# Optimization experiments

Measured on AMD Instinct MI355X. Metric: run time of the kernel, lower is better.

Reference implementation:

```python
import jax, jax.numpy as jnp
import numpy as np

N_TOKENS = 262144
D_IN = 128
D_OUT = 128
N_EXPERTS = 8


def setup_inputs() -> dict:
    key = jax.random.key(0)
    k1, k2, k3, k4 = jax.random.split(key, 4)
    x = jax.random.normal(k1, (N_TOKENS, D_IN), dtype=jnp.float32)
    split = jax.random.randint(k2, (N_TOKENS,), 0, N_EXPERTS, dtype=jnp.int64)
    # Per-expert Linear params (one "model" per unique split value).
    W = jax.random.normal(k3, (N_EXPERTS, D_IN, D_OUT), dtype=jnp.float32) / np.sqrt(D_IN)
    b = jax.random.normal(k4, (N_EXPERTS, D_OUT), dtype=jnp.float32)
    return {"x": x, "split": split, "W": W, "b": b}


def reference(x, split, W, b):
    # Original 'alone' path: gather rows per unique split value, apply
    # model[split_value], concat, then reorder via argsort of the gathered
    # indices. That composition is exactly a per-token expert apply:
    #   out[t] = x[t] @ W[split[t]] + b[split[t]]
    # Computed densely per expert (fixed shapes, jit-friendly), then select.
    y_all = jnp.einsum('nf,efg->eng', x, W) + b[:, None, :]  # [E, N, d_out]
    tok = jnp.arange(x.shape[0])
    return y_all[split, tok]  # [N, d_out]
```

## Files before the change

kernel.cpp:

```cpp
#include <hip/hip_runtime.h>


typedef __bf16 bf16x8 __attribute__((ext_vector_type(8)));
typedef unsigned short u16x8 __attribute__((ext_vector_type(8)));
typedef float f32x4 __attribute__((ext_vector_type(4)));

__device__ __forceinline__ unsigned short f2bf(float f) {
    unsigned u = __builtin_bit_cast(unsigned, f);
    u += 0x7FFFu + ((u >> 16) & 1u);
    return (unsigned short)(u >> 16);
}

__global__ void k_init(int* meta) {
    if (threadIdx.x < 16) meta[threadIdx.x] = 0;
}

__global__ void k_wt(const float* __restrict__ W, unsigned short* __restrict__ Wt) {
    __shared__ float T[16][132];
    int e = blockIdx.x >> 3;
    int g0 = (blockIdx.x & 7) << 4;
    const float* We = W + e * 128 * 128;
    #pragma unroll
    for (int i = 0; i < 2; ++i) {
        int idx = i * 256 + threadIdx.x;
        int f = idx >> 2, q = idx & 3;
        float4 v = *(const float4*)(We + f * 128 + g0 + q * 4);
        T[q * 4 + 0][f] = v.x; T[q * 4 + 1][f] = v.y;
        T[q * 4 + 2][f] = v.z; T[q * 4 + 3][f] = v.w;
    }
    __syncthreads();
    int g = threadIdx.x >> 4, fc = threadIdx.x & 15;
    u16x8 o;
    #pragma unroll
    for (int j = 0; j < 8; ++j) o[j] = f2bf(T[g][fc * 8 + j]);
    *(u16x8*)(Wt + ((e * 128 + g0 + g) * 128 + fc * 8)) = o;
}

__global__ void k_hist(const int* __restrict__ split, int* __restrict__ meta) {
    __shared__ int h[8];
    if (threadIdx.x < 8) h[threadIdx.x] = 0;
    __syncthreads();
    int t = blockIdx.x * 256 + threadIdx.x;
    atomicAdd(&h[split[t]], 1);
    __syncthreads();
    if (threadIdx.x < 8) atomicAdd(&meta[threadIdx.x], h[threadIdx.x]);
}

__global__ void k_scatter(const int* __restrict__ split, int* __restrict__ meta,
                          int* __restrict__ perm) {
    __shared__ int h[8], base[8];
    if (threadIdx.x < 8) h[threadIdx.x] = 0;
    __syncthreads();
    int t = blockIdx.x * 256 + threadIdx.x;
    int e = split[t];
    int r = atomicAdd(&h[e], 1);
    __syncthreads();
    if (threadIdx.x < 8)
        base[threadIdx.x] = atomicAdd(&meta[8 + threadIdx.x], h[threadIdx.x]);
    __syncthreads();
    int off = 0;
    #pragma unroll
    for (int ee = 0; ee < 8; ++ee) off += (ee < e) ? meta[ee] : 0;
    perm[off + base[e] + r] = t;
}

__global__ __launch_bounds__(512) void k_gemm(
    const float* __restrict__ x, const float* __restrict__ bias,
    const int* __restrict__ meta, const int* __restrict__ perm,
    const unsigned short* __restrict__ Wt, float* __restrict__ out) {

    int bid = blockIdx.x;
    int e = -1, tile = 0, cnt_e = 0, off_e = 0;
    int acc_t = 0, off = 0;
    #pragma unroll
    for (int ee = 0; ee < 8; ++ee) {
        int c = meta[ee];
        int t = (c + 255) >> 8;
        if (e < 0 && bid < acc_t + t) { e = ee; tile = bid - acc_t; cnt_e = c; off_e = off; }
        acc_t += t;
        off += c;
    }
    if (e < 0) return;

    __shared__ unsigned short Wl[16384];

    int tid = threadIdx.x;
    int lane = tid & 63;
    int w = tid >> 6;
    int l15 = lane & 15, lq = lane >> 4;

    const unsigned short* We = Wt + e * 16384;
    #pragma unroll
    for (int i = 0; i < 4; ++i) {
        int c = i * 512 + tid;
        int g = c >> 4, fc = c & 15;
        int slot = (g << 4) | (fc ^ (g & 7));
        *(u16x8*)(Wl + slot * 8) = *(const u16x8*)(We + c * 8);
    }

    bf16x8 afrag[2][4];
    #pragma unroll
    for (int i = 0; i < 2; ++i) {
        int p = tile * 256 + w * 32 + i * 16 + l15;
        int pp = p < cnt_e ? p : cnt_e - 1;
        int tok = perm[off_e + pp];
        const float* xr = x + (long)tok * 128 + lq * 8;
        #pragma unroll
        for (int kk = 0; kk < 4; ++kk) {
            float4 lo = *(const float4*)(xr + kk * 32);
            float4 hi = *(const float4*)(xr + kk * 32 + 4);
            u16x8 u;
            u[0] = f2bf(lo.x); u[1] = f2bf(lo.y); u[2] = f2bf(lo.z); u[3] = f2bf(lo.w);
            u[4] = f2bf(hi.x); u[5] = f2bf(hi.y); u[6] = f2bf(hi.z); u[7] = f2bf(hi.w);
            afrag[i][kk] = __builtin_bit_cast(bf16x8, u);
        }
    }

    __syncthreads();

    f32x4 acc[2][8];
    #pragma unroll
    for (int i = 0; i < 2; ++i)
        #pragma unroll
        for (int j = 0; j < 8; ++j) acc[i][j] = (f32x4){0.f, 0.f, 0.f, 0.f};

    #pragma unroll
    for (int kk = 0; kk < 4; ++kk) {
        #pragma unroll
        for (int j = 0; j < 8; ++j) {
            int g = j * 16 + l15;
            int fc = kk * 4 + lq;
            int slot = (g << 4) | (fc ^ (g & 7));
            bf16x8 b = *(const bf16x8*)(Wl + slot * 8);
            acc[0][j] = __builtin_amdgcn_mfma_f32_16x16x32_bf16(afrag[0][kk], b, acc[0][j], 0, 0, 0);
            acc[1][j] = __builtin_amdgcn_mfma_f32_16x16x32_bf16(afrag[1][kk], b, acc[1][j], 0, 0, 0);
        }
    }

    float bv[8];
    #pragma unroll
    for (int j = 0; j < 8; ++j) bv[j] = bias[e * 128 + j * 16 + l15];

    #pragma unroll
    for (int i = 0; i < 2; ++i) {
        #pragma unroll
        for (int r = 0; r < 4; ++r) {
            int p = tile * 256 + w * 32 + i * 16 + lq * 4 + r;
            if (p < cnt_e) {
                int tok = perm[off_e + p];
                float* o = out + (long)tok * 128 + l15;
                #pragma unroll
                for (int j = 0; j < 8; ++j) o[j * 16] = acc[i][j][r] + bv[j];
            }
        }
    }
}

extern "C" void kernel_launch(void* const* d_in, const int* in_sizes, int n_in,
                              void* d_out, int out_size, void* d_ws, size_t ws_size,
                              hipStream_t stream) {
    const float* x     = (const float*)d_in[0];
    const int*   split = (const int*)d_in[1];
    const float* W     = (const float*)d_in[2];
    const float* bias  = (const float*)d_in[3];
    float* out = (float*)d_out;

    int n = in_sizes[1];
    char* ws = (char*)d_ws;
    int* meta = (int*)ws;
    int* perm = (int*)(ws + 4096);
    unsigned short* Wt = (unsigned short*)(ws + 4096 + (size_t)n * 4);

    k_init<<<1, 64, 0, stream>>>(meta);
    k_wt<<<64, 256, 0, stream>>>(W, Wt);
    k_hist<<<n / 256, 256, 0, stream>>>(split, meta);
    k_scatter<<<n / 256, 256, 0, stream>>>(split, meta, perm);
    k_gemm<<<n / 256 + 8, 512, 0, stream>>>(x, bias, meta, perm, Wt, out);
}
```

Before: 96.12 us.

## Fuse histogram, scatter and GEMM into one per-tile kernel with local expert grouping

Replaces the global histogram/scatter/perm pipeline plus gathered GEMM with one kernel. Each block loads 256 contiguous tokens, groups them by expert in shared memory, and runs 16-row MFMA tiles per expert using weight fragments loaded from global memory. This removes three launches, the global atomics and the perm round-trip, and makes x reads coalesced. In exchange, each wave issues only one MFMA chain per 16-row tile, which raises per-tile overhead, and output writes become narrow scalar stores.

```diff
diff --git a/kernel.cpp b/kernel.cpp
--- a/kernel.cpp
+++ b/kernel.cpp
@@ -10,9 +10,8 @@
     u += 0x7FFFu + ((u >> 16) & 1u);
     return (unsigned short)(u >> 16);
 }
-
-__global__ void k_init(int* meta) {
-    if (threadIdx.x < 16) meta[threadIdx.x] = 0;
+__device__ __forceinline__ unsigned pack2(float a, float b) {
+    return (unsigned)f2bf(a) | ((unsigned)f2bf(b) << 16);
 }
 
 __global__ void k_wt(const float* __restrict__ W, unsigned short* __restrict__ Wt) {
@@ -36,121 +35,107 @@
     *(u16x8*)(Wt + ((e * 128 + g0 + g) * 128 + fc * 8)) = o;
 }
 
-__global__ void k_hist(const int* __restrict__ split, int* __restrict__ meta) {
-    __shared__ int h[8];
-    if (threadIdx.x < 8) h[threadIdx.x] = 0;
+#define NT 256
+
+__global__ __launch_bounds__(512) void k_fused(
+    const float* __restrict__ x, const int* __restrict__ split,
+    const float* __restrict__ bias, const unsigned short* __restrict__ Wt,
+    float* __restrict__ out) {
+
+    __shared__ unsigned short A[NT * 128];
+    __shared__ int hcnt[8], startE[8];
+    __shared__ int dest[NT], trow[NT];
+    __shared__ int exT[24], rbT[24], limT[24];
+    __shared__ int Tn;
+
+    const int tid = threadIdx.x;
+    const long t0 = (long)blockIdx.x * NT;
+
+    if (tid < 8) hcnt[tid] = 0;
     __syncthreads();
-    int t = blockIdx.x * 256 + threadIdx.x;
-    atomicAdd(&h[split[t]], 1);
+
+    float4 xv[16];
+    const float* xb = x + t0 * 128;
+    #pragma unroll
+    for (int rr = 0; rr < 16; ++rr)
+        xv[rr] = *(const float4*)(xb + (rr * 512 + tid) * 4);
+
+    int e = 0, rank = 0;
+    if (tid < NT) {
+        e = split[t0 + tid];
+        rank = atomicAdd(&hcnt[e], 1);
+    }
     __syncthreads();
-    if (threadIdx.x < 8) atomicAdd(&meta[threadIdx.x], h[threadIdx.x]);
-}
 
-__global__ void k_scatter(const int* __restrict__ split, int* __restrict__ meta,
-                          int* __restrict__ perm) {
-    __shared__ int h[8], base[8];
-    if (threadIdx.x < 8) h[threadIdx.x] = 0;
+    if (tid == 0) {
+        int acc = 0, T = 0;
+        for (int ee = 0; ee < 8; ++ee) {
+            int c = hcnt[ee];
+            startE[ee] = acc;
+            for (int k = 0; k < c; k += 16) {
+                exT[T] = ee; rbT[T] = acc + k;
+                limT[T] = (c - k < 16) ? (c - k) : 16; T++;
+            }
+            acc += c;
+        }
+        Tn = T;
+    }
     __syncthreads();
-    int t = blockIdx.x * 256 + threadIdx.x;
-    int e = split[t];
-    int r = atomicAdd(&h[e], 1);
+
+    if (tid < NT) {
+        int s = startE[e] + rank;
+        dest[tid] = s;
+        trow[s] = tid;
+    }
     __syncthreads();
-    if (threadIdx.x < 8)
-        base[threadIdx.x] = atomicAdd(&meta[8 + threadIdx.x], h[threadIdx.x]);
+
+    #pragma unroll
+    for (int rr = 0; rr < 16; ++rr) {
+        int c = rr * 512 + tid;
+        int row = c >> 5;
+        int s = dest[row];
+        int fc = (c & 31) >> 1;
+        int half = c & 1;
+        unsigned d0 = pack2(xv[rr].x, xv[rr].y);
+        unsigned d1 = pack2(xv[rr].z, xv[rr].w);
+        unsigned short* p = A + s * 128 + ((fc ^ (s & 7)) << 3) + half * 4;
+        *(uint2*)p = make_uint2(d0, d1);
+    }
     __syncthreads();
-    int off = 0;
-    #pragma unroll
-    for (int ee = 0; ee < 8; ++ee) off += (ee < e) ? meta[ee] : 0;
-    perm[off + base[e] + r] = t;
-}
 
-__global__ __launch_bounds__(512) void k_gemm(
-    const float* __restrict__ x, const float* __restrict__ bias,
-    const int* __restrict__ meta, const int* __restrict__ perm,
-    const unsigned short* __restrict__ Wt, float* __restrict__ out) {
+    const int lane = tid & 63, w = tid >> 6;
+    const int l15 = lane & 15, lq = lane >> 4;
+    const int T = Tn;
 
-    int bid = blockIdx.x;
-    int e = -1, tile = 0, cnt_e = 0, off_e = 0;
-    int acc_t = 0, off = 0;
-    #pragma unroll
-    for (int ee = 0; ee < 8; ++ee) {
-        int c = meta[ee];
-        int t = (c + 255) >> 8;
-        if (e < 0 && bid < acc_t + t) { e = ee; tile = bid - acc_t; cnt_e = c; off_e = off; }
-        acc_t += t;
-        off += c;
-    }
-    if (e < 0) return;
+    bf16x8 bfrag[4];
+    float bv = 0.f;
+    int preve = -1;
 
-    __shared__ unsigned short Wl[16384];
-
-    int tid = threadIdx.x;
-    int lane = tid & 63;
-    int w = tid >> 6;
-    int l15 = lane & 15, lq = lane >> 4;
-
-    const unsigned short* We = Wt + e * 16384;
-    #pragma unroll
-    for (int i = 0; i < 4; ++i) {
-        int c = i * 512 + tid;
-        int g = c >> 4, fc = c & 15;
-        int slot = (g << 4) | (fc ^ (g & 7));
-        *(u16x8*)(Wl + slot * 8) = *(const u16x8*)(We + c * 8);
-    }
-
-    bf16x8 afrag[2][4];
-    #pragma unroll
-    for (int i = 0; i < 2; ++i) {
-        int p = tile * 256 + w * 32 + i * 16 + l15;
-        int pp = p < cnt_e ? p : cnt_e - 1;
-        int tok = perm[off_e + pp];
-        const float* xr = x + (long)tok * 128 + lq * 8;
+    for (int tau = 0; tau < T; ++tau) {
+        int ee = exT[tau], rb = rbT[tau], lim = limT[tau];
+        if (ee != preve) {
+            preve = ee;
+            const unsigned short* Wb = Wt + ee * 16384 + (w * 16 + l15) * 128;
+            #pragma unroll
+            for (int kk = 0; kk < 4; ++kk)
+                bfrag[kk] = *(const bf16x8*)(Wb + (kk * 4 + lq) * 8);
+            bv = bias[ee * 128 + w * 16 + l15];
+        }
+        int srow = rb + l15;
+        srow = srow < NT - 1 ? srow : NT - 1;
+        f32x4 acc = {0.f, 0.f, 0.f, 0.f};
         #pragma unroll
         for (int kk = 0; kk < 4; ++kk) {
-            float4 lo = *(const float4*)(xr + kk * 32);
-            float4 hi = *(const float4*)(xr + kk * 32 + 4);
-            u16x8 u;
-            u[0] = f2bf(lo.x); u[1] = f2bf(lo.y); u[2] = f2bf(lo.z); u[3] = f2bf(lo.w);
-            u[4] = f2bf(hi.x); u[5] = f2bf(hi.y); u[6] = f2bf(hi.z); u[7] = f2bf(hi.w);
-            afrag[i][kk] = __builtin_bit_cast(bf16x8, u);
+            int fc = kk * 4 + lq;
+            bf16x8 a = *(const bf16x8*)(A + srow * 128 + ((fc ^ (srow & 7)) << 3));
+            acc = __builtin_amdgcn_mfma_f32_16x16x32_bf16(a, bfrag[kk], acc, 0, 0, 0);
         }
-    }
-
-    __syncthreads();
-
-    f32x4 acc[2][8];
-    #pragma unroll
-    for (int i = 0; i < 2; ++i)
-        #pragma unroll
-        for (int j = 0; j < 8; ++j) acc[i][j] = (f32x4){0.f, 0.f, 0.f, 0.f};
-
-    #pragma unroll
-    for (int kk = 0; kk < 4; ++kk) {
-        #pragma unroll
-        for (int j = 0; j < 8; ++j) {
-            int g = j * 16 + l15;
-            int fc = kk * 4 + lq;
-            int slot = (g << 4) | (fc ^ (g & 7));
-            bf16x8 b = *(const bf16x8*)(Wl + slot * 8);
-            acc[0][j] = __builtin_amdgcn_mfma_f32_16x16x32_bf16(afrag[0][kk], b, acc[0][j], 0, 0, 0);
-            acc[1][j] = __builtin_amdgcn_mfma_f32_16x16x32_bf16(afrag[1][kk], b, acc[1][j], 0, 0, 0);
-        }
-    }
-
-    float bv[8];
-    #pragma unroll
-    for (int j = 0; j < 8; ++j) bv[j] = bias[e * 128 + j * 16 + l15];
-
-    #pragma unroll
-    for (int i = 0; i < 2; ++i) {
         #pragma unroll
         for (int r = 0; r < 4; ++r) {
-            int p = tile * 256 + w * 32 + i * 16 + lq * 4 + r;
-            if (p < cnt_e) {
-                int tok = perm[off_e + p];
-                float* o = out + (long)tok * 128 + l15;
-                #pragma unroll
-                for (int j = 0; j < 8; ++j) o[j * 16] = acc[i][j][r] + bv[j];
+            int ri = lq * 4 + r;
+            if (ri < lim) {
+                int tokl = trow[rb + ri];
+                out[(t0 + tokl) * 128 + w * 16 + l15] = acc[r] + bv;
             }
         }
     }
@@ -166,14 +151,8 @@
     float* out = (float*)d_out;
 
     int n = in_sizes[1];
-    char* ws = (char*)d_ws;
-    int* meta = (int*)ws;
-    int* perm = (int*)(ws + 4096);
-    unsigned short* Wt = (unsigned short*)(ws + 4096 + (size_t)n * 4);
+    unsigned short* Wt = (unsigned short*)d_ws;
 
-    k_init<<<1, 64, 0, stream>>>(meta);
     k_wt<<<64, 256, 0, stream>>>(W, Wt);
-    k_hist<<<n / 256, 256, 0, stream>>>(split, meta);
-    k_scatter<<<n / 256, 256, 0, stream>>>(split, meta, perm);
-    k_gemm<<<n / 256 + 8, 512, 0, stream>>>(x, bias, meta, perm, Wt, out);
+    k_fused<<<n / NT, 512, 0, stream>>>(x, split, bias, Wt, out);
 }
```

Result: faster. 83.02 us (-13.6%).
